# Kernel optimization log

Hardware: AMD Instinct MI355X
Metric: run time of the kernel (lower is better)

## Reference

```python
import jax, jax.numpy as jnp
import numpy as np
import math

BBOX_XFORM_CLIP = math.log(1000.0 / 16.0)  # standard BoxCoder clip on dw/dh
WX, WY, WW, WH = 10.0, 10.0, 5.0, 5.0      # BoxCoder weights
TO_REMOVE = 1.0                             # legacy +1 box convention


def _decode(rel_codes, boxes):
    # boxes: [N,4] xyxy reference proposals; rel_codes: [N,4] deltas
    widths = boxes[:, 2] - boxes[:, 0] + TO_REMOVE
    heights = boxes[:, 3] - boxes[:, 1] + TO_REMOVE
    ctr_x = boxes[:, 0] + 0.5 * widths
    ctr_y = boxes[:, 1] + 0.5 * heights

    dx = rel_codes[:, 0] / WX
    dy = rel_codes[:, 1] / WY
    dw = jnp.minimum(rel_codes[:, 2] / WW, BBOX_XFORM_CLIP)
    dh = jnp.minimum(rel_codes[:, 3] / WH, BBOX_XFORM_CLIP)

    pred_ctr_x = dx * widths + ctr_x
    pred_ctr_y = dy * heights + ctr_y
    pred_w = jnp.exp(dw) * widths
    pred_h = jnp.exp(dh) * heights

    x1 = pred_ctr_x - 0.5 * pred_w
    y1 = pred_ctr_y - 0.5 * pred_h
    x2 = pred_ctr_x + 0.5 * pred_w - 1.0
    y2 = pred_ctr_y + 0.5 * pred_h - 1.0
    return jnp.stack([x1, y1, x2, y2], axis=1)


def setup_inputs() -> dict:
    key = jax.random.key(0)
    k1, k2, k3, k4 = jax.random.split(key, 4)
    N, C = 262144, 81
    W = H = 1024
    class_logits = jax.random.normal(k1, (N, C), dtype=jnp.float32)
    box_regression = jax.random.normal(k2, (N, 4), dtype=jnp.float32) * 0.5
    # valid xyxy proposals inside the image: x2 > x1, y2 > y1
    xy1 = jax.random.uniform(k3, (N, 2), dtype=jnp.float32) * (W - 64.0)
    wh = jax.random.uniform(k4, (N, 2), dtype=jnp.float32) * 60.0 + 2.0
    proposal_boxes = jnp.concatenate([xy1, xy1 + wh], axis=1)
    return {
        "class_logits": class_logits,
        "box_regression": box_regression,
        "proposal_boxes": proposal_boxes,
        "img_w": W,
        "img_h": H,
    }


def reference(class_logits, box_regression, proposal_boxes, img_w, img_h):
    # softmax over classes
    class_prob = jax.nn.softmax(class_logits, axis=-1)  # [N, C]
    rel = box_regression[:, -4:]
    proposals = _decode(rel, proposal_boxes)            # [N, 4]
    proposals = jnp.maximum(proposals, 0.0)             # proposals[proposals < 0] = 0
    C = class_prob.shape[1]
    # is_repeat path: repeat decoded box for every class, then per-row boxlist
    boxes = jnp.tile(proposals, (1, C)).reshape(-1, 4)  # [N*C, 4]
    # clip_to_image (remove_empty=False): clamp to [0, W-1] x [0, H-1]
    wmax = jnp.asarray(img_w - 1, dtype=boxes.dtype)
    hmax = jnp.asarray(img_h - 1, dtype=boxes.dtype)
    x1 = jnp.clip(boxes[:, 0], 0.0, wmax)
    y1 = jnp.clip(boxes[:, 1], 0.0, hmax)
    x2 = jnp.clip(boxes[:, 2], 0.0, wmax)
    y2 = jnp.clip(boxes[:, 3], 0.0, hmax)
    boxes = jnp.stack([x1, y1, x2, y2], axis=1)         # [N*C, 4]
    scores = class_prob.reshape(-1)                     # [N*C]
    return boxes, scores
```

## Files before the change

### kernel.cpp

```cpp
#include <hip/hip_runtime.h>
#include <math.h>

#define NUM_CLASSES 81
#define ROWS_PER_BLOCK 16
#define ELEMS_PER_BLOCK (ROWS_PER_BLOCK * NUM_CLASSES)
#define VEC_PER_BLOCK   (ELEMS_PER_BLOCK / 4)

typedef float vfloat4 __attribute__((ext_vector_type(4)));

__global__ __launch_bounds__(256) void fused_kernel(
    const float* __restrict__ logits,
    const float4* __restrict__ box_reg4,
    const float4* __restrict__ prop4,
    const int* __restrict__ img_w_p,
    const int* __restrict__ img_h_p,
    float* __restrict__ out_boxes,
    float* __restrict__ out_scores,
    int N)
{
    __shared__ vfloat4 lds4[VEC_PER_BLOCK];
    float* lds_val = (float*)lds4;
    __shared__ float4 lds_box[ROWS_PER_BLOCK];

    const int tid = threadIdx.x;
    const int block_row0 = blockIdx.x * ROWS_PER_BLOCK;
    if (block_row0 >= N) return;
    const int rows  = min(ROWS_PER_BLOCK, N - block_row0);
    const bool full = (rows == ROWS_PER_BLOCK);
    const int elems = rows * NUM_CLASSES;

    const float* lbase = logits + (size_t)block_row0 * NUM_CLASSES;
    if (full) {
        const vfloat4* lbase4 = (const vfloat4*)lbase;
        { int idx = tid;        if (true)               lds4[idx] = lbase4[idx]; }
        { int idx = tid + 256;  if (idx < VEC_PER_BLOCK) lds4[idx] = lbase4[idx]; }
    } else {
        for (int i = 0; i < 6; ++i) {
            int e = tid + i * 256;
            if (e < elems) lds_val[e] = lbase[e];
        }
    }

    if (tid < rows) {
        const int row = block_row0 + tid;
        const float4 b = prop4[row];
        const float4 r = box_reg4[row];
        const float wmax = (float)(*img_w_p) - 1.0f;
        const float hmax = (float)(*img_h_p) - 1.0f;

        const float BBOX_XFORM_CLIP = 4.135166556742356f;
        const float w  = b.z - b.x + 1.0f;
        const float h  = b.w - b.y + 1.0f;
        const float cx = b.x + 0.5f * w;
        const float cy = b.y + 0.5f * h;
        const float dx = r.x * 0.1f;
        const float dy = r.y * 0.1f;
        const float dw = fminf(r.z * 0.2f, BBOX_XFORM_CLIP);
        const float dh = fminf(r.w * 0.2f, BBOX_XFORM_CLIP);
        const float px = dx * w + cx;
        const float py = dy * h + cy;
        const float pw = expf(dw) * w;
        const float ph = expf(dh) * h;
        const float x1 = fminf(fmaxf(px - 0.5f * pw, 0.0f), wmax);
        const float y1 = fminf(fmaxf(py - 0.5f * ph, 0.0f), hmax);
        const float x2 = fminf(fmaxf(px + 0.5f * pw - 1.0f, 0.0f), wmax);
        const float y2 = fminf(fmaxf(py + 0.5f * ph - 1.0f, 0.0f), hmax);
        lds_box[tid] = make_float4(x1, y1, x2, y2);
    }
    __syncthreads();

    const int sub = tid & 15;
    const int rl  = tid >> 4;
    if (rl < rows) {
        float* rowv = lds_val + rl * NUM_CLASSES;

        float v[6];
        float m = -INFINITY;
        #pragma unroll
        for (int i = 0; i < 6; ++i) {
            const int k = sub + i * 16;
            if (k < NUM_CLASSES) { v[i] = rowv[k]; m = fmaxf(m, v[i]); }
            else                 { v[i] = -INFINITY; }
        }
        #pragma unroll
        for (int off = 1; off <= 8; off <<= 1)
            m = fmaxf(m, __shfl_xor(m, off));

        float s = 0.0f;
        #pragma unroll
        for (int i = 0; i < 6; ++i) {
            const int k = sub + i * 16;
            if (k < NUM_CLASSES) { v[i] = __expf(v[i] - m); s += v[i]; }
        }
        #pragma unroll
        for (int off = 1; off <= 8; off <<= 1)
            s += __shfl_xor(s, off);

        const float inv = 1.0f / s;
        #pragma unroll
        for (int i = 0; i < 6; ++i) {
            const int k = sub + i * 16;
            if (k < NUM_CLASSES) rowv[k] = v[i] * inv;
        }
    }
    __syncthreads();

    const size_t sbase = (size_t)block_row0 * NUM_CLASSES;

    if (full) {
        vfloat4* sdst4 = (vfloat4*)(out_scores + sbase);
        { int idx = tid;       __builtin_nontemporal_store(lds4[idx], sdst4 + idx); }
        { int idx = tid + 256; if (idx < VEC_PER_BLOCK)
                               __builtin_nontemporal_store(lds4[idx], sdst4 + idx); }

        vfloat4* bdst4 = (vfloat4*)(out_boxes + sbase * 4);
        #pragma unroll
        for (int i = 0; i < 6; ++i) {
            const int j = tid + i * 256;
            if (i < 5 || j < ELEMS_PER_BLOCK) {
                const int r = (int)(((unsigned)j * 12946u) >> 20);
                const float4 bx = lds_box[r];
                vfloat4 bv = { bx.x, bx.y, bx.z, bx.w };
                __builtin_nontemporal_store(bv, bdst4 + j);
            }
        }
    } else {
        float* sdst = out_scores + sbase;
        for (int i = 0; i < 6; ++i) {
            int e = tid + i * 256;
            if (e < elems) sdst[e] = lds_val[e];
        }
        float4* bdst = (float4*)(out_boxes + sbase * 4);
        for (int i = 0; i < 6; ++i) {
            int j = tid + i * 256;
            if (j < elems) {
                const int r = (int)(((unsigned)j * 12946u) >> 20);
                bdst[j] = lds_box[r];
            }
        }
    }
}

extern "C" void kernel_launch(void* const* d_in, const int* in_sizes, int n_in,
                              void* d_out, int out_size, void* d_ws, size_t ws_size,
                              hipStream_t stream) {
    const float* logits   = (const float*)d_in[0];
    const float4* boxreg4 = (const float4*)d_in[1];
    const float4* prop4   = (const float4*)d_in[2];
    const int*   img_w_p  = (const int*)d_in[3];
    const int*   img_h_p  = (const int*)d_in[4];

    const int N = in_sizes[1] / 4;

    float* out_boxes  = (float*)d_out;
    float* out_scores = out_boxes + (size_t)N * NUM_CLASSES * 4;

    const int blocks = (N + ROWS_PER_BLOCK - 1) / ROWS_PER_BLOCK;
    fused_kernel<<<blocks, 256, 0, stream>>>(
        logits, boxreg4, prop4, img_w_p, img_h_p, out_boxes, out_scores, N);
}
```

Measured before the change: 488.8 us.

## Split fused kernel into separate box-broadcast and softmax-score kernels

```diff
diff --git a/kernel.cpp b/kernel.cpp
--- a/kernel.cpp
+++ b/kernel.cpp
@@ -2,70 +2,117 @@
 #include <math.h>
 
 #define NUM_CLASSES 81
-#define ROWS_PER_BLOCK 16
-#define ELEMS_PER_BLOCK (ROWS_PER_BLOCK * NUM_CLASSES)
-#define VEC_PER_BLOCK   (ELEMS_PER_BLOCK / 4)
 
 typedef float vfloat4 __attribute__((ext_vector_type(4)));
 
-__global__ __launch_bounds__(256) void fused_kernel(
-    const float* __restrict__ logits,
+__device__ __forceinline__ float4 decode_clip(const float4 b, const float4 r,
+                                              const float wmax, const float hmax)
+{
+    const float BBOX_XFORM_CLIP = 4.135166556742356f;
+    const float w  = b.z - b.x + 1.0f;
+    const float h  = b.w - b.y + 1.0f;
+    const float cx = b.x + 0.5f * w;
+    const float cy = b.y + 0.5f * h;
+    const float dx = r.x * 0.1f;
+    const float dy = r.y * 0.1f;
+    const float dw = fminf(r.z * 0.2f, BBOX_XFORM_CLIP);
+    const float dh = fminf(r.w * 0.2f, BBOX_XFORM_CLIP);
+    const float px = dx * w + cx;
+    const float py = dy * h + cy;
+    const float pw = expf(dw) * w;
+    const float ph = expf(dh) * h;
+    const float x1 = fminf(fmaxf(px - 0.5f * pw, 0.0f), wmax);
+    const float y1 = fminf(fmaxf(py - 0.5f * ph, 0.0f), hmax);
+    const float x2 = fminf(fmaxf(px + 0.5f * pw - 1.0f, 0.0f), wmax);
+    const float y2 = fminf(fmaxf(py + 0.5f * ph - 1.0f, 0.0f), hmax);
+    return make_float4(x1, y1, x2, y2);
+}
+
+#define BROWS  64
+#define BELEMS (BROWS * NUM_CLASSES)
+#define BITERS (BELEMS / 256)
+
+__global__ __launch_bounds__(256) void boxes_kernel(
     const float4* __restrict__ box_reg4,
     const float4* __restrict__ prop4,
     const int* __restrict__ img_w_p,
     const int* __restrict__ img_h_p,
     float* __restrict__ out_boxes,
+    int N)
+{
+    __shared__ float4 lds_box[BROWS];
+    const int tid  = threadIdx.x;
+    const int row0 = blockIdx.x * BROWS;
+    if (row0 >= N) return;
+    const int rows = min(BROWS, N - row0);
+
+    if (tid < rows) {
+        const int row = row0 + tid;
+        const float wmax = (float)(*img_w_p) - 1.0f;
+        const float hmax = (float)(*img_h_p) - 1.0f;
+        lds_box[tid] = decode_clip(prop4[row], box_reg4[row], wmax, hmax);
+    }
+    __syncthreads();
+
+    vfloat4* dst = (vfloat4*)out_boxes + (size_t)row0 * NUM_CLASSES;
+    if (rows == BROWS) {
+        #pragma unroll
+        for (int i = 0; i < BITERS; ++i) {
+            const int j = tid + i * 256;
+            const int rloc = (int)(((unsigned)j * 12946u) >> 20);
+            const float4 bx = lds_box[rloc];
+            vfloat4 bv = { bx.x, bx.y, bx.z, bx.w };
+            __builtin_nontemporal_store(bv, dst + j);
+        }
+        if (tid < (BELEMS - BITERS * 256)) {
+            const int j = BITERS * 256 + tid;
+            const int rloc = (int)(((unsigned)j * 12946u) >> 20);
+            const float4 bx = lds_box[rloc];
+            vfloat4 bv = { bx.x, bx.y, bx.z, bx.w };
+            __builtin_nontemporal_store(bv, dst + j);
+        }
+    } else {
+        const int elems = rows * NUM_CLASSES;
+        for (int i = 0; i <= BITERS; ++i) {
+            const int j = tid + i * 256;
+            if (j < elems) {
+                const int rloc = (int)(((unsigned)j * 12946u) >> 20);
+                const float4 bx = lds_box[rloc];
+                vfloat4 bv = { bx.x, bx.y, bx.z, bx.w };
+                __builtin_nontemporal_store(bv, dst + j);
+            }
+        }
+    }
+}
+
+#define SROWS  16
+#define SELEMS (SROWS * NUM_CLASSES)
+#define SVECS  (SELEMS / 4)
+
+__global__ __launch_bounds__(256) void scores_kernel(
+    const float* __restrict__ logits,
     float* __restrict__ out_scores,
     int N)
 {
-    __shared__ vfloat4 lds4[VEC_PER_BLOCK];
+    __shared__ vfloat4 lds4[SVECS];
     float* lds_val = (float*)lds4;
-    __shared__ float4 lds_box[ROWS_PER_BLOCK];
-
-    const int tid = threadIdx.x;
-    const int block_row0 = blockIdx.x * ROWS_PER_BLOCK;
-    if (block_row0 >= N) return;
-    const int rows  = min(ROWS_PER_BLOCK, N - block_row0);
-    const bool full = (rows == ROWS_PER_BLOCK);
+    const int tid  = threadIdx.x;
+    const int row0 = blockIdx.x * SROWS;
+    if (row0 >= N) return;
+    const int rows = min(SROWS, N - row0);
+    const bool full = (rows == SROWS);
     const int elems = rows * NUM_CLASSES;
 
-    const float* lbase = logits + (size_t)block_row0 * NUM_CLASSES;
+    const float* lbase = logits + (size_t)row0 * NUM_CLASSES;
     if (full) {
         const vfloat4* lbase4 = (const vfloat4*)lbase;
-        { int idx = tid;        if (true)               lds4[idx] = lbase4[idx]; }
-        { int idx = tid + 256;  if (idx < VEC_PER_BLOCK) lds4[idx] = lbase4[idx]; }
+        { int idx = tid;        lds4[idx] = lbase4[idx]; }
+        { int idx = tid + 256;  if (idx < SVECS) lds4[idx] = lbase4[idx]; }
     } else {
         for (int i = 0; i < 6; ++i) {
             int e = tid + i * 256;
             if (e < elems) lds_val[e] = lbase[e];
         }
-    }
-
-    if (tid < rows) {
-        const int row = block_row0 + tid;
-        const float4 b = prop4[row];
-        const float4 r = box_reg4[row];
-        const float wmax = (float)(*img_w_p) - 1.0f;
-        const float hmax = (float)(*img_h_p) - 1.0f;
-
-        const float BBOX_XFORM_CLIP = 4.135166556742356f;
-        const float w  = b.z - b.x + 1.0f;
-        const float h  = b.w - b.y + 1.0f;
-        const float cx = b.x + 0.5f * w;
-        const float cy = b.y + 0.5f * h;
-        const float dx = r.x * 0.1f;
-        const float dy = r.y * 0.1f;
-        const float dw = fminf(r.z * 0.2f, BBOX_XFORM_CLIP);
-        const float dh = fminf(r.w * 0.2f, BBOX_XFORM_CLIP);
-        const float px = dx * w + cx;
-        const float py = dy * h + cy;
-        const float pw = expf(dw) * w;
-        const float ph = expf(dh) * h;
-        const float x1 = fminf(fmaxf(px - 0.5f * pw, 0.0f), wmax);
-        const float y1 = fminf(fmaxf(py - 0.5f * ph, 0.0f), hmax);
-        const float x2 = fminf(fmaxf(px + 0.5f * pw - 1.0f, 0.0f), wmax);
-        const float y2 = fminf(fmaxf(py + 0.5f * ph - 1.0f, 0.0f), hmax);
-        lds_box[tid] = make_float4(x1, y1, x2, y2);
     }
     __syncthreads();
 
@@ -105,38 +152,16 @@
     }
     __syncthreads();
 
-    const size_t sbase = (size_t)block_row0 * NUM_CLASSES;
-
+    float* sdst = out_scores + (size_t)row0 * NUM_CLASSES;
     if (full) {
-        vfloat4* sdst4 = (vfloat4*)(out_scores + sbase);
+        vfloat4* sdst4 = (vfloat4*)sdst;
         { int idx = tid;       __builtin_nontemporal_store(lds4[idx], sdst4 + idx); }
-        { int idx = tid + 256; if (idx < VEC_PER_BLOCK)
+        { int idx = tid + 256; if (idx < SVECS)
                                __builtin_nontemporal_store(lds4[idx], sdst4 + idx); }
-
-        vfloat4* bdst4 = (vfloat4*)(out_boxes + sbase * 4);
-        #pragma unroll
-        for (int i = 0; i < 6; ++i) {
-            const int j = tid + i * 256;
-            if (i < 5 || j < ELEMS_PER_BLOCK) {
-                const int r = (int)(((unsigned)j * 12946u) >> 20);
-                const float4 bx = lds_box[r];
-                vfloat4 bv = { bx.x, bx.y, bx.z, bx.w };
-                __builtin_nontemporal_store(bv, bdst4 + j);
-            }
-        }
     } else {
-        float* sdst = out_scores + sbase;
         for (int i = 0; i < 6; ++i) {
             int e = tid + i * 256;
             if (e < elems) sdst[e] = lds_val[e];
-        }
-        float4* bdst = (float4*)(out_boxes + sbase * 4);
-        for (int i = 0; i < 6; ++i) {
-            int j = tid + i * 256;
-            if (j < elems) {
-                const int r = (int)(((unsigned)j * 12946u) >> 20);
-                bdst[j] = lds_box[r];
-            }
         }
     }
 }
@@ -155,7 +180,10 @@
     float* out_boxes  = (float*)d_out;
     float* out_scores = out_boxes + (size_t)N * NUM_CLASSES * 4;
 
-    const int blocks = (N + ROWS_PER_BLOCK - 1) / ROWS_PER_BLOCK;
-    fused_kernel<<<blocks, 256, 0, stream>>>(
-        logits, boxreg4, prop4, img_w_p, img_h_p, out_boxes, out_scores, N);
+    const int bblocks = (N + BROWS - 1) / BROWS;
+    boxes_kernel<<<bblocks, 256, 0, stream>>>(
+        boxreg4, prop4, img_w_p, img_h_p, out_boxes, N);
+
+    const int sblocks = (N + SROWS - 1) / SROWS;
+    scores_kernel<<<sblocks, 256, 0, stream>>>(logits, out_scores, N);
 }
```

Measured after the change: 483.6 us, median of 2. Within noise of the previous version (-1.1%).
